# Kernel optimization log

Measured on AMD Instinct MI355X. Metric: run time of the kernel, lower is better.

Reference implementation:

```python
import jax, jax.numpy as jnp
import numpy as np

BN_EPS = 1e-5
K2 = 9  # 3x3 kernel


def _conv3x3(x, w, b):
    # x: [B,C,H,W], w: [O,C,3,3] -> [B,O,H,W], stride 1, pad 1
    out = jax.lax.conv_general_dilated(
        x, w, window_strides=(1, 1), padding=((1, 1), (1, 1)),
        dimension_numbers=("NCHW", "OIHW", "NCHW"))
    return out + b[None, :, None, None]


def setup_inputs() -> dict:
    key = jax.random.key(0)
    ks = jax.random.split(key, 8)
    B, C, H, W = 8, 256, 64, 64
    O = 256
    x = jax.random.normal(ks[0], (B, C, H, W), dtype=jnp.float32)
    # offset/mask conv: small init so sampled offsets stay near the base grid
    w_off = jax.random.normal(ks[1], (3 * K2, C, 3, 3), dtype=jnp.float32) * 0.01
    b_off = jnp.zeros((3 * K2,), dtype=jnp.float32)
    weight = jax.random.normal(ks[2], (O, C, 3, 3), dtype=jnp.float32) * 0.02
    bias = jnp.zeros((O,), dtype=jnp.float32)
    gamma = jnp.ones((O,), dtype=jnp.float32)
    beta = jnp.zeros((O,), dtype=jnp.float32)
    run_mean = jax.random.normal(ks[3], (O,), dtype=jnp.float32) * 0.1
    run_var = jax.random.uniform(ks[4], (O,), dtype=jnp.float32) + 0.5
    return {"x": x, "w_off": w_off, "b_off": b_off, "weight": weight,
            "bias": bias, "gamma": gamma, "beta": beta,
            "run_mean": run_mean, "run_var": run_var}


def _deform_sample(img, py, px):
    # img: [C,H,W]; py, px: [K2,H,W] sampling coordinates.
    # Bilinear sample with zero padding outside (DCNv2 semantics:
    # out-of-bounds corners contribute zero).
    C, H, W = img.shape
    y0 = jnp.floor(py)
    x0 = jnp.floor(px)
    wy1 = py - y0  # frac weights for the 'high' corner
    wx1 = px - x0

    def gather(yi, xi):
        valid = (yi >= 0) & (yi < H) & (xi >= 0) & (xi < W)
        yc = jnp.clip(yi, 0, H - 1).astype(jnp.int32)
        xc = jnp.clip(xi, 0, W - 1).astype(jnp.int32)
        return img[:, yc, xc] * valid.astype(img.dtype)[None]  # [C,K2,H,W]

    v00 = gather(y0, x0)
    v01 = gather(y0, x0 + 1)
    v10 = gather(y0 + 1, x0)
    v11 = gather(y0 + 1, x0 + 1)
    return (v00 * ((1 - wy1) * (1 - wx1))[None]
            + v01 * ((1 - wy1) * wx1)[None]
            + v10 * (wy1 * (1 - wx1))[None]
            + v11 * (wy1 * wx1)[None])  # [C,K2,H,W]


def reference(x, w_off, b_off, weight, bias, gamma, beta, run_mean, run_var):
    B, C, H, W = x.shape
    O = weight.shape[0]
    # 1) offset / mask branch (standard 3x3 conv)
    om = _conv3x3(x, w_off, b_off)  # [B, 27, H, W]
    off_y = om[:, :K2]
    off_x = om[:, K2:2 * K2]
    mask = jax.nn.sigmoid(om[:, 2 * K2:])  # modulation, [B,9,H,W]
    # 2) base sampling grid for 3x3, stride 1, pad 1, dilation 1
    ky = jnp.repeat(jnp.arange(3), 3).astype(x.dtype)  # [9]
    kx = jnp.tile(jnp.arange(3), 3).astype(x.dtype)    # [9]
    hs = jnp.arange(H, dtype=x.dtype)
    ws = jnp.arange(W, dtype=x.dtype)
    base_y = hs[None, :, None] - 1.0 + ky[:, None, None]  # [9,H,1]
    base_x = ws[None, None, :] - 1.0 + kx[:, None, None]  # [9,1,W]
    py = base_y[None] + off_y  # [B,9,H,W]
    px = base_x[None] + off_x
    # 3) modulated deformable im2col (bilinear gather) per batch
    cols = jax.vmap(_deform_sample)(x, py, px)  # [B,C,9,H,W]
    cols = cols * mask[:, None]                 # apply modulation mask
    # 4) GEMM over (C, K2) + bias
    w3 = weight.reshape(O, C, K2)
    out = jnp.einsum("ock,bckhw->bohw", w3, cols) + bias[None, :, None, None]
    # 5) BatchNorm (eval mode, running stats) + ReLU
    inv = gamma / jnp.sqrt(run_var + BN_EPS)
    out = out * inv[None, :, None, None] + (beta - run_mean * inv)[None, :, None, None]
    return jax.nn.relu(out)
```

## Files before the change

kernel.cpp:

```cpp
#include <hip/hip_runtime.h>
#include <math.h>

#define H 64
#define W 64
#define C 256
#define O 256
#define CK 2304
#define NB 8
#define HWSZ 4096

typedef __attribute__((ext_vector_type(8))) short short8;
typedef __attribute__((ext_vector_type(4))) float floatx4;
typedef __attribute__((ext_vector_type(4))) unsigned uintx4;

#define FSWZ(n) ((((n) & 3) << 1) | (((n) >> 2) & 1))

__device__ __forceinline__ float lo2f(unsigned u) {
  return __builtin_bit_cast(float, u << 16);
}
__device__ __forceinline__ float hi2f(unsigned u) {
  return __builtin_bit_cast(float, u & 0xffff0000u);
}
__device__ __forceinline__ unsigned pk2bf(float v0, float v1) {
  unsigned a = __builtin_bit_cast(unsigned, v0);
  unsigned b = __builtin_bit_cast(unsigned, v1);
  return ((a + 0x8000u) >> 16) | ((b + 0x8000u) & 0xffff0000u);
}
__device__ __forceinline__ unsigned cvtpk(float v0, float v1) {
#if defined(__gfx950__) && __has_builtin(__builtin_amdgcn_cvt_pk_bf16_f32)
  typedef __attribute__((ext_vector_type(2))) __bf16 bf16x2;
  bf16x2 t = __builtin_amdgcn_cvt_pk_bf16_f32(v0, v1);
  return __builtin_bit_cast(unsigned, t);
#else
  return pk2bf(v0, v1);
#endif
}

__global__ __launch_bounds__(256) void prep_all(
    const float* __restrict__ x, const float* __restrict__ weight,
    const float* __restrict__ w_off, const float* __restrict__ bias,
    const float* __restrict__ gamma, const float* __restrict__ beta,
    const float* __restrict__ run_mean, const float* __restrict__ run_var,
    unsigned short* __restrict__ xt, unsigned short* __restrict__ wb,
    unsigned short* __restrict__ wob, float* __restrict__ invsh) {
  __shared__ unsigned tile[64 * 65];
  int bid = blockIdx.x;
  int tid = threadIdx.x;

  if (bid < 1024) {
    int b = bid & 7;
    int t = bid >> 3;
    int y = t >> 1;
    int cg = t & 1;
    const float* xb = x + ((size_t)b * C + cg * 128) * HWSZ + y * W;
#pragma unroll
    for (int it = 0; it < 4; ++it) {
      int e = tid + 256 * it;
      int xx4 = e & 15;
      int cp = e >> 4;
      floatx4 f0 = *reinterpret_cast<const floatx4*>(
          xb + (size_t)(2 * cp) * HWSZ + xx4 * 4);
      floatx4 f1 = *reinterpret_cast<const floatx4*>(
          xb + (size_t)(2 * cp + 1) * HWSZ + xx4 * 4);
#pragma unroll
      for (int k = 0; k < 4; ++k)
        tile[cp * 65 + xx4 * 4 + k] = cvtpk(f0[k], f1[k]);
    }
    __syncthreads();
    unsigned short* xo = xt + ((size_t)(b * 64 + y) << 14) + cg * 128;
#pragma unroll
    for (int it = 0; it < 4; ++it) {
      int e = tid + 256 * it;
      int cq = e & 15;
      int xx = e >> 4;
      unsigned u0 = tile[(cq * 4 + 0) * 65 + xx];
      unsigned u1 = tile[(cq * 4 + 1) * 65 + xx];
      unsigned u2 = tile[(cq * 4 + 2) * 65 + xx];
      unsigned u3 = tile[(cq * 4 + 3) * 65 + xx];
      uint4 v = {u0, u1, u2, u3};
      *reinterpret_cast<uint4*>(xo + (xx << 8) + (cq << 3)) = v;
    }
  } else if (bid < 1312) {
    int d0 = ((bid - 1024) * 256 + tid) * 8;
    int lane = (d0 >> 3) & 63;
    int mt = (d0 >> 9) & 15;
    int ks = d0 >> 13;
    int o = mt * 16 + (lane & 15);
    int kn0 = ks * 32 + (lane >> 4) * 8;
    int tap = kn0 >> 8;
    int c0 = kn0 & 255;
    const float* wsrc = weight + o * CK + c0 * 9 + tap;
    unsigned pk[4];
#pragma unroll
    for (int p = 0; p < 4; ++p)
      pk[p] = cvtpk(wsrc[(2 * p) * 9], wsrc[(2 * p + 1) * 9]);
    uint4 v = {pk[0], pk[1], pk[2], pk[3]};
    *reinterpret_cast<uint4*>(wb + d0) = v;
  } else if (bid < 1348) {
    int d0 = ((bid - 1312) * 256 + tid) * 8;
    int lane = (d0 >> 3) & 63;
    int mt = (d0 >> 9) & 1;
    int ks = d0 >> 10;
    int o = mt * 16 + (lane & 15);
    int kn0 = ks * 32 + (lane >> 4) * 8;
    int tap = kn0 >> 8;
    int c0 = kn0 & 255;
    uint4 v;
    if (o < 27) {
      const float* wsrc = w_off + o * CK + c0 * 9 + tap;
      unsigned pk[4];
#pragma unroll
      for (int p = 0; p < 4; ++p)
        pk[p] = cvtpk(wsrc[(2 * p) * 9], wsrc[(2 * p + 1) * 9]);
      v = (uint4){pk[0], pk[1], pk[2], pk[3]};
    } else {
      v = (uint4){0, 0, 0, 0};
    }
    *reinterpret_cast<uint4*>(wob + d0) = v;
  } else {
    int o = tid;
    float inv = gamma[o] * rsqrtf(run_var[o] + 1e-5f);
    invsh[o] = inv;
    invsh[O + o] = beta[o] + (bias[o] - run_mean[o]) * inv;
  }
}

__global__ __launch_bounds__(512, 4) void deform_mfma_kernel(
    const unsigned short* __restrict__ xt, const unsigned short* __restrict__ wob,
    const float* __restrict__ b_off, const unsigned short* __restrict__ wb,
    const float* __restrict__ invsh, float* __restrict__ out) {
  __shared__ short cols[64 * 256];
  __shared__ float sm_om[27 * 64];
  __shared__ int sbase[576];
  __shared__ float s00[576], s01[576], s10[576], s11[576];

  int tid = threadIdx.x;
  int lane = tid & 63;
  int wvid = tid >> 6;
  int q = lane >> 4;
  int lm = lane & 15;
  int b = blockIdx.x;
  int h = blockIdx.y;
  const unsigned short* xtb = xt + ((size_t)b << 20);

  {
    int mt = wvid & 1;
    int nt = wvid >> 1;
    floatx4 a0 = (floatx4){0.f, 0.f, 0.f, 0.f};
    int px = nt * 16 + lm;
    for (int tap = 0; tap < 9; ++tap) {
      int yy = h - 1 + tap / 3;
      int xx = px - 1 + tap % 3;
      bool v = (yy >= 0) && (yy < H) && (xx >= 0) && (xx < W);
      const unsigned short* bp =
          xtb + ((((yy & 63) << 6) + (xx & 63)) << 8) + q * 8;
#pragma unroll
      for (int s = 0; s < 8; ++s) {
        int ks = tap * 8 + s;
        short8 bfrag;
        if (v)
          bfrag = *reinterpret_cast<const short8*>(bp + s * 32);
        else
          bfrag = (short8){0, 0, 0, 0, 0, 0, 0, 0};
        short8 afrag = *reinterpret_cast<const short8*>(
            wob + (((ks * 2 + mt) * 64 + lane) << 3));
        a0 = __builtin_amdgcn_mfma_f32_16x16x32_bf16(afrag, bfrag, a0, 0, 0, 0);
      }
    }
#pragma unroll
    for (int r = 0; r < 4; ++r) {
      int o = mt * 16 + q * 4 + r;
      if (o < 27) sm_om[o * 64 + px] = a0[r] + b_off[o];
    }
  }
  __syncthreads();

  for (int e = tid; e < 576; e += 512) {
    int n = e & 63;
    int k = e >> 6;
    float oy = sm_om[k * 64 + n];
    float ox = sm_om[(9 + k) * 64 + n];
    float mv = sm_om[(18 + k) * 64 + n];
    float m = 1.0f / (1.0f + __expf(-mv));
    float py = (float)(h - 1 + k / 3) + oy;
    float px = (float)(n - 1 + k % 3) + ox;
    float yf = floorf(py), xf = floorf(px);
    int y0 = (int)yf, x0 = (int)xf;
    float fy = py - yf, fx = px - xf;
    float r0, r1; int yl;
    if (y0 >= 0 && y0 <= H - 2)      { yl = y0;    r0 = 1.f - fy; r1 = fy;       }
    else if (y0 == -1)               { yl = 0;     r0 = fy;       r1 = 0.f;      }
    else if (y0 == H - 1)            { yl = H - 2; r0 = 0.f;      r1 = 1.f - fy; }
    else                             { yl = 0;     r0 = 0.f;      r1 = 0.f;      }
    float c0, c1; int xl;
    if (x0 >= 0 && x0 <= W - 2)      { xl = x0;    c0 = 1.f - fx; c1 = fx;       }
    else if (x0 == -1)               { xl = 0;     c0 = fx;       c1 = 0.f;      }
    else if (x0 == W - 1)            { xl = W - 2; c0 = 0.f;      c1 = 1.f - fx; }
    else                             { xl = 0;     c0 = 0.f;      c1 = 0.f;      }
    r0 *= m; r1 *= m;
    sbase[e] = ((yl << 6) + xl) << 8;
    s00[e] = r0 * c0; s01[e] = r0 * c1;
    s10[e] = r1 * c0; s11[e] = r1 * c1;
  }
  __syncthreads();

  floatx4 acc[2][4];
#pragma unroll
  for (int a = 0; a < 2; ++a)
#pragma unroll
    for (int u = 0; u < 4; ++u) acc[a][u] = (floatx4){0.f, 0.f, 0.f, 0.f};

  int sn = tid >> 3;
  int scb = tid & 7;

  uintx4 pf00[2], pf01[2], pf10[2], pf11[2];
  {
    const unsigned short* p0 = xtb + sbase[sn];
#pragma unroll
    for (int i = 0; i < 2; ++i) {
      int co = ((i << 3) | scb) << 3;
      pf00[i] = *reinterpret_cast<const uintx4*>(p0 + co);
      pf01[i] = *reinterpret_cast<const uintx4*>(p0 + 256 + co);
      pf10[i] = *reinterpret_cast<const uintx4*>(p0 + 16384 + co);
      pf11[i] = *reinterpret_cast<const uintx4*>(p0 + 16640 + co);
    }
  }

  for (int tap = 0; tap < 9; ++tap) {
    int ei = tap * 64 + sn;
    float w00 = s00[ei], w01 = s01[ei], w10 = s10[ei], w11 = s11[ei];
    const unsigned short* p = xtb + sbase[ei];

    uintx4 t00[2], t01[2], t10[2], t11[2];
#pragma unroll
    for (int i = 0; i < 2; ++i) {
      int co = (((i + 2) << 3) | scb) << 3;
      t00[i] = *reinterpret_cast<const uintx4*>(p + co);
      t01[i] = *reinterpret_cast<const uintx4*>(p + 256 + co);
      t10[i] = *reinterpret_cast<const uintx4*>(p + 16384 + co);
      t11[i] = *reinterpret_cast<const uintx4*>(p + 16640 + co);
    }
#pragma unroll
    for (int i = 0; i < 2; ++i) {
      int cbw = (i << 3) | scb;
      uintx4 res;
#pragma unroll
      for (int jd = 0; jd < 4; ++jd) {
        float v0 = fmaf(w00, lo2f(pf00[i][jd]),
                   fmaf(w01, lo2f(pf01[i][jd]),
                   fmaf(w10, lo2f(pf10[i][jd]), w11 * lo2f(pf11[i][jd]))));
        float v1 = fmaf(w00, hi2f(pf00[i][jd]),
                   fmaf(w01, hi2f(pf01[i][jd]),
                   fmaf(w10, hi2f(pf10[i][jd]), w11 * hi2f(pf11[i][jd]))));
        res[jd] = cvtpk(v0, v1);
      }
      int pos = (cbw ^ FSWZ(sn)) & 31;
      *reinterpret_cast<uintx4*>(&cols[(sn << 8) + (pos << 3)]) = res;
    }
#pragma unroll
    for (int i = 0; i < 2; ++i) {
      int cbw = ((i + 2) << 3) | scb;
      uintx4 res;
#pragma unroll
      for (int jd = 0; jd < 4; ++jd) {
        float v0 = fmaf(w00, lo2f(t00[i][jd]),
                   fmaf(w01, lo2f(t01[i][jd]),
                   fmaf(w10, lo2f(t10[i][jd]), w11 * lo2f(t11[i][jd]))));
        float v1 = fmaf(w00, hi2f(t00[i][jd]),
                   fmaf(w01, hi2f(t01[i][jd]),
                   fmaf(w10, hi2f(t10[i][jd]), w11 * hi2f(t11[i][jd]))));
        res[jd] = cvtpk(v0, v1);
      }
      int pos = (cbw ^ FSWZ(sn)) & 31;
      *reinterpret_cast<uintx4*>(&cols[(sn << 8) + (pos << 3)]) = res;
    }
    __syncthreads();

    if (tap < 8) {
      const unsigned short* pn = xtb + sbase[ei + 64];
#pragma unroll
      for (int i = 0; i < 2; ++i) {
        int co = ((i << 3) | scb) << 3;
        pf00[i] = *reinterpret_cast<const uintx4*>(pn + co);
        pf01[i] = *reinterpret_cast<const uintx4*>(pn + 256 + co);
        pf10[i] = *reinterpret_cast<const uintx4*>(pn + 16384 + co);
        pf11[i] = *reinterpret_cast<const uintx4*>(pn + 16640 + co);
      }
    }

#pragma unroll
    for (int s = 0; s < 8; ++s) {
      int ks = tap * 8 + s;
      short8 afrag[2];
#pragma unroll
      for (int a = 0; a < 2; ++a)
        afrag[a] = *reinterpret_cast<const short8*>(
            wb + (((ks * 16 + wvid * 2 + a) * 64 + lane) << 3));
      short8 bfrag[4];
#pragma unroll
      for (int u = 0; u < 4; ++u) {
        int nn = u * 16 + lm;
        int pos = ((s * 4 + q) ^ FSWZ(nn)) & 31;
        bfrag[u] = *reinterpret_cast<const short8*>(&cols[(nn << 8) + (pos << 3)]);
      }
#pragma unroll
      for (int a = 0; a < 2; ++a)
#pragma unroll
        for (int u = 0; u < 4; ++u)
          acc[a][u] = __builtin_amdgcn_mfma_f32_16x16x32_bf16(
              afrag[a], bfrag[u], acc[a][u], 0, 0, 0);
    }
    __syncthreads();
  }

#pragma unroll
  for (int a = 0; a < 2; ++a) {
#pragma unroll
    for (int u = 0; u < 4; ++u) {
      int nn = u * 16 + lm;
#pragma unroll
      for (int r = 0; r < 4; ++r) {
        int o = (wvid * 2 + a) * 16 + q * 4 + r;
        float v = fmaf(acc[a][u][r], invsh[o], invsh[O + o]);
        out[((size_t)(b * O + o)) * HWSZ + h * W + nn] = fmaxf(v, 0.0f);
      }
    }
  }
}

extern "C" void kernel_launch(void* const* d_in, const int* in_sizes, int n_in,
                              void* d_out, int out_size, void* d_ws, size_t ws_size,
                              hipStream_t stream) {
  const float* x        = (const float*)d_in[0];
  const float* w_off    = (const float*)d_in[1];
  const float* b_off    = (const float*)d_in[2];
  const float* weight   = (const float*)d_in[3];
  const float* bias     = (const float*)d_in[4];
  const float* gamma    = (const float*)d_in[5];
  const float* beta     = (const float*)d_in[6];
  const float* run_mean = (const float*)d_in[7];
  const float* run_var  = (const float*)d_in[8];
  float* out = (float*)d_out;

  char* ws = (char*)d_ws;
  unsigned short* xt = (unsigned short*)ws;
  unsigned short* wbf = (unsigned short*)(ws + 16777216);
  unsigned short* wob = (unsigned short*)(ws + 17956864);
  float* invsh = (float*)(ws + 18104320);

  prep_all<<<1349, 256, 0, stream>>>(x, weight, w_off, bias, gamma, beta,
                                     run_mean, run_var, xt, wbf, wob, invsh);
  {
    dim3 grid(NB, H);
    deform_mfma_kernel<<<grid, 512, 0, stream>>>(xt, wob, b_off, wbf, invsh, out);
  }
}
```

Before: 209.9 us.

## Split each tap into channel halves with double-buffered LDS and one barrier

```diff
diff --git a/kernel.cpp b/kernel.cpp
--- a/kernel.cpp
+++ b/kernel.cpp
@@ -13,7 +13,7 @@
 typedef __attribute__((ext_vector_type(4))) float floatx4;
 typedef __attribute__((ext_vector_type(4))) unsigned uintx4;
 
-#define FSWZ(n) ((((n) & 3) << 1) | (((n) >> 2) & 1))
+#define FS(n) ((((n) & 7) << 1) | (((n) >> 3) & 1))
 
 __device__ __forceinline__ float lo2f(unsigned u) {
   return __builtin_bit_cast(float, u << 16);
@@ -125,11 +125,11 @@
   }
 }
 
-__global__ __launch_bounds__(512, 4) void deform_mfma_kernel(
+__global__ __launch_bounds__(512, 2) void deform_mfma_kernel(
     const unsigned short* __restrict__ xt, const unsigned short* __restrict__ wob,
     const float* __restrict__ b_off, const unsigned short* __restrict__ wb,
     const float* __restrict__ invsh, float* __restrict__ out) {
-  __shared__ short cols[64 * 256];
+  __shared__ short cols[2 * 64 * 128];
   __shared__ float sm_om[27 * 64];
   __shared__ int sbase[576];
   __shared__ float s00[576], s01[576], s10[576], s11[576];
@@ -226,23 +226,15 @@
     }
   }
 
-  for (int tap = 0; tap < 9; ++tap) {
+  for (int ht = 0; ht < 18; ++ht) {
+    int tap = ht >> 1;
+    int half = ht & 1;
     int ei = tap * 64 + sn;
     float w00 = s00[ei], w01 = s01[ei], w10 = s10[ei], w11 = s11[ei];
-    const unsigned short* p = xtb + sbase[ei];
-
-    uintx4 t00[2], t01[2], t10[2], t11[2];
+    short* cbuf = &cols[(ht & 1) << 13];
+
 #pragma unroll
     for (int i = 0; i < 2; ++i) {
-      int co = (((i + 2) << 3) | scb) << 3;
-      t00[i] = *reinterpret_cast<const uintx4*>(p + co);
-      t01[i] = *reinterpret_cast<const uintx4*>(p + 256 + co);
-      t10[i] = *reinterpret_cast<const uintx4*>(p + 16384 + co);
-      t11[i] = *reinterpret_cast<const uintx4*>(p + 16640 + co);
-    }
-#pragma unroll
-    for (int i = 0; i < 2; ++i) {
-      int cbw = (i << 3) | scb;
       uintx4 res;
 #pragma unroll
       for (int jd = 0; jd < 4; ++jd) {
@@ -254,33 +246,20 @@
                    fmaf(w10, hi2f(pf10[i][jd]), w11 * hi2f(pf11[i][jd]))));
         res[jd] = cvtpk(v0, v1);
       }
-      int pos = (cbw ^ FSWZ(sn)) & 31;
-      *reinterpret_cast<uintx4*>(&cols[(sn << 8) + (pos << 3)]) = res;
-    }
-#pragma unroll
-    for (int i = 0; i < 2; ++i) {
-      int cbw = ((i + 2) << 3) | scb;
-      uintx4 res;
-#pragma unroll
-      for (int jd = 0; jd < 4; ++jd) {
-        float v0 = fmaf(w00, lo2f(t00[i][jd]),
-                   fmaf(w01, lo2f(t01[i][jd]),
-                   fmaf(w10, lo2f(t10[i][jd]), w11 * lo2f(t11[i][jd]))));
-        float v1 = fmaf(w00, hi2f(t00[i][jd]),
-                   fmaf(w01, hi2f(t01[i][jd]),
-                   fmaf(w10, hi2f(t10[i][jd]), w11 * hi2f(t11[i][jd]))));
-        res[jd] = cvtpk(v0, v1);
-      }
-      int pos = (cbw ^ FSWZ(sn)) & 31;
-      *reinterpret_cast<uintx4*>(&cols[(sn << 8) + (pos << 3)]) = res;
+      int cb4 = (i << 3) | scb;
+      int pos = (cb4 ^ FS(sn)) & 15;
+      *reinterpret_cast<uintx4*>(&cbuf[(sn << 7) + (pos << 3)]) = res;
     }
     __syncthreads();
 
-    if (tap < 8) {
-      const unsigned short* pn = xtb + sbase[ei + 64];
+    if (ht < 17) {
+      int htn = ht + 1;
+      int tapn = htn >> 1;
+      int halfn = htn & 1;
+      const unsigned short* pn = xtb + sbase[tapn * 64 + sn];
 #pragma unroll
       for (int i = 0; i < 2; ++i) {
-        int co = ((i << 3) | scb) << 3;
+        int co = ((halfn << 4) | (i << 3) | scb) << 3;
         pf00[i] = *reinterpret_cast<const uintx4*>(pn + co);
         pf01[i] = *reinterpret_cast<const uintx4*>(pn + 256 + co);
         pf10[i] = *reinterpret_cast<const uintx4*>(pn + 16384 + co);
@@ -289,7 +268,8 @@
     }
 
 #pragma unroll
-    for (int s = 0; s < 8; ++s) {
+    for (int sl = 0; sl < 4; ++sl) {
+      int s = half * 4 + sl;
       int ks = tap * 8 + s;
       short8 afrag[2];
 #pragma unroll
@@ -300,8 +280,9 @@
 #pragma unroll
       for (int u = 0; u < 4; ++u) {
         int nn = u * 16 + lm;
-        int pos = ((s * 4 + q) ^ FSWZ(nn)) & 31;
-        bfrag[u] = *reinterpret_cast<const short8*>(&cols[(nn << 8) + (pos << 3)]);
+        int cb4 = (sl << 2) | q;
+        int pos = (cb4 ^ FS(nn)) & 15;
+        bfrag[u] = *reinterpret_cast<const short8*>(&cbuf[(nn << 7) + (pos << 3)]);
       }
 #pragma unroll
       for (int a = 0; a < 2; ++a)
@@ -310,7 +291,6 @@
           acc[a][u] = __builtin_amdgcn_mfma_f32_16x16x32_bf16(
               afrag[a], bfrag[u], acc[a][u], 0, 0, 0);
     }
-    __syncthreads();
   }
 
 #pragma unroll
```

Result: faster. 195.4 us (-6.9%).
